# Kernel tuning notes

Measured on AMD Instinct MI355X. Metric: run time of the kernel, lower is better.

Reference implementation:

```python
import jax, jax.numpy as jnp
import numpy as np

EMB = 1024

def setup_inputs() -> dict:
    key = jax.random.key(0)
    ks = jax.random.split(key, 10)
    B, S, E = 8, 2048, EMB
    x = jax.random.normal(ks[0], (B, S, E), dtype=jnp.float32)
    context = jax.random.normal(ks[1], (B, S, E), dtype=jnp.float32)
    pad_mask = jax.random.randint(ks[2], (B, S, S), 0, 2) == 1
    s = 1.0 / np.sqrt(E)
    Wq = jax.random.normal(ks[3], (E, E), dtype=jnp.float32) * s
    bq = jnp.zeros((E,), dtype=jnp.float32)
    Wk = jax.random.normal(ks[4], (E, E), dtype=jnp.float32) * s
    bk = jnp.zeros((E,), dtype=jnp.float32)
    Wv = jax.random.normal(ks[5], (E, E), dtype=jnp.float32) * s
    bv = jnp.zeros((E,), dtype=jnp.float32)
    return {"x": x, "context": context, "pad_mask": pad_mask,
            "Wq": Wq, "bq": bq, "Wk": Wk, "bk": bk, "Wv": Wv, "bv": bv}

def reference(x, context, pad_mask, Wq, bq, Wk, bk, Wv, bv):
    scale = x.shape[-1] ** (-0.5)
    Q = jnp.einsum('bse,fe->bsf', x, Wq) + bq
    K = jnp.einsum('bse,fe->bsf', context, Wk) + bk
    V = jnp.einsum('bse,fe->bsf', context, Wv) + bv
    att = jnp.einsum('bid,bjd->bij', Q, K) * scale
    att = jnp.where(pad_mask, jnp.float32(-1e9), att)
    att = jax.nn.softmax(att, axis=-1)
    out = jnp.einsum('bij,bjk->bik', att, V)
    return (out, att)
```

## Files before the change

kernel.cpp:

```cpp
#include <hip/hip_runtime.h>
#include <hip/hip_bf16.h>
#include <type_traits>

typedef __attribute__((ext_vector_type(8))) __bf16 bf16x8;
typedef __attribute__((ext_vector_type(4))) float f32x4;
typedef unsigned short u16;

__device__ __forceinline__ u16 f2b(float x) {
  union { __hip_bfloat16 b; u16 u; } cv;
  cv.b = __float2bfloat16(x);
  return cv.u;
}

__device__ __forceinline__ void ld16(const u16* g, u16* l) {
  __builtin_amdgcn_global_load_lds(
      (const __attribute__((address_space(1))) unsigned int*)g,
      (__attribute__((address_space(3))) unsigned int*)l, 16, 0, 0);
}

constexpr int BM = 256, BN = 256, BK = 64;

enum { EPI_NONE = 0, EPI_BIAS = 1, EPI_BIAS_T = 2 };

#define PHASE(QR, QC, LA, LB, BUF)                                            \
  {                                                                           \
    if (LA) {                                                                 \
      _Pragma("unroll") for (int i = 0; i < 4; ++i)                           \
          _Pragma("unroll") for (int ks = 0; ks < 2; ++ks)                    \
              aF[i][ks] = *(const bf16x8*)&As[BUF][                           \
                  (wr * 128 + QR * 64 + i * 16 + fr) * BK +                   \
                  (((ks * 4 + quad) ^ (fr & 7)) * 8)];                        \
    }                                                                         \
    if (LB) {                                                                 \
      _Pragma("unroll") for (int j = 0; j < 2; ++j)                           \
          _Pragma("unroll") for (int ks = 0; ks < 2; ++ks)                    \
              bF[j][ks] = *(const bf16x8*)&Bs[BUF][                           \
                  (wc * 64 + QC * 32 + j * 16 + fr) * BK +                    \
                  (((ks * 4 + quad) ^ (fr & 7)) * 8)];                        \
    }                                                                         \
    _Pragma("unroll") for (int i = 0; i < 4; ++i)                             \
        _Pragma("unroll") for (int j = 0; j < 2; ++j)                         \
            _Pragma("unroll") for (int ks = 0; ks < 2; ++ks)                  \
                acc[QR * 4 + i][QC * 2 + j] =                                 \
                    __builtin_amdgcn_mfma_f32_16x16x32_bf16(                  \
                        aF[i][ks], bF[j][ks], acc[QR * 4 + i][QC * 2 + j],    \
                        0, 0, 0);                                             \
  }

template <typename TC, int EPI>
__global__ __launch_bounds__(512, 2) void gemm_bt(
    const u16* __restrict__ A, const u16* __restrict__ Bt, TC* __restrict__ C,
    const float* __restrict__ bias, float scale, int N, int K, long long sA,
    long long sB, long long sC) {
  __shared__ u16 As[2][BM * BK];
  __shared__ u16 Bs[2][BN * BK];

  const int gx = gridDim.x, gy = gridDim.y;
  const int nwg = gx * gy * gridDim.z;
  int flat = (blockIdx.z * gy + blockIdx.y) * gx + blockIdx.x;
  flat = (flat & 7) * (nwg >> 3) + (flat >> 3);
  const int bx = flat % gx;
  const int rem = flat / gx;
  const int by = rem % gy;
  const int bz = rem / gy;

  A += (size_t)bz * sA;
  Bt += (size_t)bz * sB;
  C += (size_t)bz * sC;

  const int m0 = by * BM, n0 = bx * BN;
  const int t = threadIdx.x, wave = t >> 6, lane = t & 63;
  const int wr = wave >> 2, wc = wave & 3;
  const int fr = lane & 15, quad = lane >> 4;
  const int lr = lane >> 3, lc = lane & 7;

  const u16* ga = A + (size_t)(m0 + wave * 8 + lr) * K + (lc ^ lr) * 8;
  const u16* gb = Bt + (size_t)(n0 + wave * 8 + lr) * K + (lc ^ lr) * 8;

  f32x4 acc[8][4] = {};
  bf16x8 aF[4][2], bF[2][2];

  const int nt = K / BK;

  auto STAGE = [&](int kt, int bsel) {
    const size_t ko = (size_t)kt * BK;
#pragma unroll
    for (int i = 0; i < 4; ++i) {
      ld16(ga + (size_t)(i * 64) * K + ko,
           &As[bsel][(i * 64 + wave * 8) * BK]);
      ld16(gb + (size_t)(i * 64) * K + ko,
           &Bs[bsel][(i * 64 + wave * 8) * BK]);
    }
  };

  STAGE(0, 0);
  STAGE(1, 1);

  for (int kt = 0; kt < nt; ++kt) {
    const int b = kt & 1;
    if (kt + 1 < nt)
      __builtin_amdgcn_s_waitcnt(0x0f78);
    else
      __builtin_amdgcn_s_waitcnt(0x0f70);
    __builtin_amdgcn_s_barrier();
    __builtin_amdgcn_sched_barrier(0);

    PHASE(0, 0, 1, 1, b)
    PHASE(0, 1, 0, 1, b)
    PHASE(1, 1, 1, 0, b)
    PHASE(1, 0, 0, 1, b)

    __builtin_amdgcn_sched_barrier(0);
    __builtin_amdgcn_s_barrier();
    if (kt + 2 < nt) STAGE(kt + 2, b);
  }

#pragma unroll
  for (int i = 0; i < 8; ++i)
#pragma unroll
    for (int j = 0; j < 4; ++j) {
      const int mb = m0 + wr * 128 + i * 16 + quad * 4;
      const int n = n0 + wc * 64 + j * 16 + fr;
      if constexpr (EPI == EPI_BIAS_T) {
        const float bb = bias[n];
        const int b = mb >> 11, ml = mb & 2047;
        ushort4 o;
        o.x = f2b(acc[i][j][0] + bb);
        o.y = f2b(acc[i][j][1] + bb);
        o.z = f2b(acc[i][j][2] + bb);
        o.w = f2b(acc[i][j][3] + bb);
        *(ushort4*)&((u16*)C)[(size_t)b * 2097152 + (size_t)n * 2048 + ml] = o;
      } else {
#pragma unroll
        for (int r = 0; r < 4; ++r) {
          const int m = mb + r;
          float v = acc[i][j][r];
          if constexpr (EPI == EPI_BIAS) v += bias[n];
          if constexpr (std::is_same_v<TC, u16>)
            C[(size_t)m * N + n] = f2b(v);
          else
            C[(size_t)m * N + n] = v;
        }
      }
    }
}

__global__ __launch_bounds__(256) void cast_all(
    const float* __restrict__ x, const float* __restrict__ ctx,
    const float* __restrict__ wq, const float* __restrict__ wk,
    const float* __restrict__ wv, u16* __restrict__ xb, u16* __restrict__ cb,
    u16* __restrict__ wqb, u16* __restrict__ wkb, u16* __restrict__ wvb) {
  int b = blockIdx.x;
  const float* s;
  u16* d;
  size_t off;
  if (b < 16384) { s = x; d = xb; off = b; }
  else if (b < 32768) { s = ctx; d = cb; off = b - 32768 + 16384; }
  else if (b < 33792) { s = wq; d = wqb; off = b - 32768; }
  else if (b < 34816) { s = wk; d = wkb; off = b - 33792; }
  else { s = wv; d = wvb; off = b - 34816; }
  const size_t i = (off * 256 + threadIdx.x) * 4;
  float4 v = *(const float4*)&s[i];
  ushort4 h;
  h.x = f2b(v.x); h.y = f2b(v.y); h.z = f2b(v.z); h.w = f2b(v.w);
  *(ushort4*)&d[i] = h;
}

__device__ __forceinline__ float blockReduceMax(float v, float* red) {
#pragma unroll
  for (int o = 32; o > 0; o >>= 1) v = fmaxf(v, __shfl_down(v, o));
  int t = threadIdx.x;
  if ((t & 63) == 0) red[t >> 6] = v;
  __syncthreads();
  float r = fmaxf(fmaxf(red[0], red[1]), fmaxf(red[2], red[3]));
  __syncthreads();
  return r;
}

__device__ __forceinline__ float blockReduceSum(float v, float* red) {
#pragma unroll
  for (int o = 32; o > 0; o >>= 1) v += __shfl_down(v, o);
  int t = threadIdx.x;
  if ((t & 63) == 0) red[t >> 6] = v;
  __syncthreads();
  float r = red[0] + red[1] + red[2] + red[3];
  __syncthreads();
  return r;
}

__global__ __launch_bounds__(256) void softmax_rows(float* __restrict__ att,
                                                    u16* __restrict__ attb,
                                                    const int* __restrict__ msk,
                                                    float scale) {
  __shared__ float red[4];
  float* p = att + (size_t)blockIdx.x * 2048;
  const int* mr = msk + (size_t)blockIdx.x * 2048;
  u16* pb = attb + (size_t)blockIdx.x * 2048;
  const int t = threadIdx.x;
  float4 v0 = ((const float4*)p)[t];
  float4 v1 = ((const float4*)p)[t + 256];
  int4 q0 = ((const int4*)mr)[t];
  int4 q1 = ((const int4*)mr)[t + 256];
  v0.x = q0.x ? -1e9f : v0.x * scale;
  v0.y = q0.y ? -1e9f : v0.y * scale;
  v0.z = q0.z ? -1e9f : v0.z * scale;
  v0.w = q0.w ? -1e9f : v0.w * scale;
  v1.x = q1.x ? -1e9f : v1.x * scale;
  v1.y = q1.y ? -1e9f : v1.y * scale;
  v1.z = q1.z ? -1e9f : v1.z * scale;
  v1.w = q1.w ? -1e9f : v1.w * scale;
  float mx = fmaxf(fmaxf(fmaxf(v0.x, v0.y), fmaxf(v0.z, v0.w)),
                   fmaxf(fmaxf(v1.x, v1.y), fmaxf(v1.z, v1.w)));
  mx = blockReduceMax(mx, red);
  float4 e0, e1;
  e0.x = __expf(v0.x - mx); e0.y = __expf(v0.y - mx);
  e0.z = __expf(v0.z - mx); e0.w = __expf(v0.w - mx);
  e1.x = __expf(v1.x - mx); e1.y = __expf(v1.y - mx);
  e1.z = __expf(v1.z - mx); e1.w = __expf(v1.w - mx);
  float s = (e0.x + e0.y + e0.z + e0.w) + (e1.x + e1.y + e1.z + e1.w);
  s = blockReduceSum(s, red);
  float inv = 1.0f / s;
  e0.x *= inv; e0.y *= inv; e0.z *= inv; e0.w *= inv;
  e1.x *= inv; e1.y *= inv; e1.z *= inv; e1.w *= inv;
  ((float4*)p)[t] = e0;
  ((float4*)p)[t + 256] = e1;
  ushort4 h0, h1;
  h0.x = f2b(e0.x); h0.y = f2b(e0.y); h0.z = f2b(e0.z); h0.w = f2b(e0.w);
  h1.x = f2b(e1.x); h1.y = f2b(e1.y); h1.z = f2b(e1.z); h1.w = f2b(e1.w);
  *(ushort4*)&pb[(size_t)t * 4] = h0;
  *(ushort4*)&pb[(size_t)(t + 256) * 4] = h1;
}

extern "C" void kernel_launch(void* const* d_in, const int* in_sizes, int n_in,
                              void* d_out, int out_size, void* d_ws,
                              size_t ws_size, hipStream_t stream) {
  const float* x   = (const float*)d_in[0];
  const float* ctx = (const float*)d_in[1];
  const int*   msk = (const int*)d_in[2];
  const float* Wq  = (const float*)d_in[3];
  const float* bq  = (const float*)d_in[4];
  const float* Wk  = (const float*)d_in[5];
  const float* bk  = (const float*)d_in[6];
  const float* Wv  = (const float*)d_in[7];
  const float* bv  = (const float*)d_in[8];

  float* out = (float*)d_out;
  float* att = out + 16777216;

  u16* xb = (u16*)d_ws;
  u16* cb = xb + 16777216;
  u16* Q  = cb + 16777216;
  u16* Kb = Q + 16777216;
  u16* Vt = xb;
  u16* attb = Q;
  u16* wqb = (u16*)att;
  u16* wkb = wqb + 1048576;
  u16* wvb = wkb + 1048576;

  dim3 blk(256), blkg(512);
  const long long SQ = 2048LL * 1024, SS = 2048LL * 2048, SV = 1024LL * 2048;

  cast_all<<<dim3(35840), blk, 0, stream>>>(x, ctx, Wq, Wk, Wv, xb, cb, wqb,
                                            wkb, wvb);

  gemm_bt<u16, EPI_BIAS><<<dim3(4, 64, 1), blkg, 0, stream>>>(
      xb, wqb, Q, bq, 0.f, 1024, 1024, 0, 0, 0);
  gemm_bt<u16, EPI_BIAS><<<dim3(4, 64, 1), blkg, 0, stream>>>(
      cb, wkb, Kb, bk, 0.f, 1024, 1024, 0, 0, 0);
  gemm_bt<u16, EPI_BIAS_T><<<dim3(4, 64, 1), blkg, 0, stream>>>(
      cb, wvb, Vt, bv, 0.f, 1024, 1024, 0, 0, 0);

  gemm_bt<float, EPI_NONE><<<dim3(8, 8, 8), blkg, 0, stream>>>(
      Q, Kb, att, nullptr, 0.f, 2048, 1024, SQ, SQ, SS);

  softmax_rows<<<dim3(16384), blk, 0, stream>>>(att, attb, msk, 0.03125f);

  gemm_bt<float, EPI_NONE><<<dim3(4, 8, 8), blkg, 0, stream>>>(
      attb, Vt, out, nullptr, 0.f, 1024, 2048, SS, SV, SQ);
}
```

Baseline: 682.2 us.

## Restructure GEMM inner loop into two halves and batch Q/K projections

Replaces the four-phase fragment schedule with two halves: all B fragments and the first half of A are loaded, MFMAs run, the second half of A is read, and the next tile's global-to-LDS stage is issued before the second MFMA half. This lets the prefetch overlap compute rather than wait until the end of the iteration. Q and K projections are merged into one launch using the z dimension, with a per-batch bias selector. More B fragments are held in registers, which raises register pressure.

```diff
diff --git a/kernel.cpp b/kernel.cpp
--- a/kernel.cpp
+++ b/kernel.cpp
@@ -22,36 +22,11 @@
 
 enum { EPI_NONE = 0, EPI_BIAS = 1, EPI_BIAS_T = 2 };
 
-#define PHASE(QR, QC, LA, LB, BUF)                                            \
-  {                                                                           \
-    if (LA) {                                                                 \
-      _Pragma("unroll") for (int i = 0; i < 4; ++i)                           \
-          _Pragma("unroll") for (int ks = 0; ks < 2; ++ks)                    \
-              aF[i][ks] = *(const bf16x8*)&As[BUF][                           \
-                  (wr * 128 + QR * 64 + i * 16 + fr) * BK +                   \
-                  (((ks * 4 + quad) ^ (fr & 7)) * 8)];                        \
-    }                                                                         \
-    if (LB) {                                                                 \
-      _Pragma("unroll") for (int j = 0; j < 2; ++j)                           \
-          _Pragma("unroll") for (int ks = 0; ks < 2; ++ks)                    \
-              bF[j][ks] = *(const bf16x8*)&Bs[BUF][                           \
-                  (wc * 64 + QC * 32 + j * 16 + fr) * BK +                    \
-                  (((ks * 4 + quad) ^ (fr & 7)) * 8)];                        \
-    }                                                                         \
-    _Pragma("unroll") for (int i = 0; i < 4; ++i)                             \
-        _Pragma("unroll") for (int j = 0; j < 2; ++j)                         \
-            _Pragma("unroll") for (int ks = 0; ks < 2; ++ks)                  \
-                acc[QR * 4 + i][QC * 2 + j] =                                 \
-                    __builtin_amdgcn_mfma_f32_16x16x32_bf16(                  \
-                        aF[i][ks], bF[j][ks], acc[QR * 4 + i][QC * 2 + j],    \
-                        0, 0, 0);                                             \
-  }
-
 template <typename TC, int EPI>
 __global__ __launch_bounds__(512, 2) void gemm_bt(
     const u16* __restrict__ A, const u16* __restrict__ Bt, TC* __restrict__ C,
-    const float* __restrict__ bias, float scale, int N, int K, long long sA,
-    long long sB, long long sC) {
+    const float* __restrict__ bias, const float* __restrict__ bias2, int N,
+    int K, long long sA, long long sB, long long sC) {
   __shared__ u16 As[2][BM * BK];
   __shared__ u16 Bs[2][BN * BK];
 
@@ -67,6 +42,7 @@
   A += (size_t)bz * sA;
   Bt += (size_t)bz * sB;
   C += (size_t)bz * sC;
+  const float* bsel = (bz == 0) ? bias : bias2;
 
   const int m0 = by * BM, n0 = bx * BN;
   const int t = threadIdx.x, wave = t >> 6, lane = t & 63;
@@ -78,18 +54,18 @@
   const u16* gb = Bt + (size_t)(n0 + wave * 8 + lr) * K + (lc ^ lr) * 8;
 
   f32x4 acc[8][4] = {};
-  bf16x8 aF[4][2], bF[2][2];
+  bf16x8 aF[4][2], bF[4][2];
 
   const int nt = K / BK;
 
-  auto STAGE = [&](int kt, int bsel) {
+  auto STAGE = [&](int kt, int bsel2) {
     const size_t ko = (size_t)kt * BK;
 #pragma unroll
     for (int i = 0; i < 4; ++i) {
       ld16(ga + (size_t)(i * 64) * K + ko,
-           &As[bsel][(i * 64 + wave * 8) * BK]);
+           &As[bsel2][(i * 64 + wave * 8) * BK]);
       ld16(gb + (size_t)(i * 64) * K + ko,
-           &Bs[bsel][(i * 64 + wave * 8) * BK]);
+           &Bs[bsel2][(i * 64 + wave * 8) * BK]);
     }
   };
 
@@ -105,14 +81,48 @@
     __builtin_amdgcn_s_barrier();
     __builtin_amdgcn_sched_barrier(0);
 
-    PHASE(0, 0, 1, 1, b)
-    PHASE(0, 1, 0, 1, b)
-    PHASE(1, 1, 1, 0, b)
-    PHASE(1, 0, 0, 1, b)
-
+#pragma unroll
+    for (int i = 0; i < 4; ++i)
+#pragma unroll
+      for (int ks = 0; ks < 2; ++ks)
+        aF[i][ks] = *(const bf16x8*)&As[b][
+            (wr * 128 + i * 16 + fr) * BK + (((ks * 4 + quad) ^ (fr & 7)) * 8)];
+#pragma unroll
+    for (int j = 0; j < 4; ++j)
+#pragma unroll
+      for (int ks = 0; ks < 2; ++ks)
+        bF[j][ks] = *(const bf16x8*)&Bs[b][
+            (wc * 64 + j * 16 + fr) * BK + (((ks * 4 + quad) ^ (fr & 7)) * 8)];
+#pragma unroll
+    for (int i = 0; i < 4; ++i)
+#pragma unroll
+      for (int j = 0; j < 4; ++j)
+#pragma unroll
+        for (int ks = 0; ks < 2; ++ks)
+          acc[i][j] = __builtin_amdgcn_mfma_f32_16x16x32_bf16(
+              aF[i][ks], bF[j][ks], acc[i][j], 0, 0, 0);
+
+#pragma unroll
+    for (int i = 0; i < 4; ++i)
+#pragma unroll
+      for (int ks = 0; ks < 2; ++ks)
+        aF[i][ks] = *(const bf16x8*)&As[b][
+            (wr * 128 + 64 + i * 16 + fr) * BK +
+            (((ks * 4 + quad) ^ (fr & 7)) * 8)];
+    __builtin_amdgcn_s_waitcnt(0xc07f);
     __builtin_amdgcn_sched_barrier(0);
     __builtin_amdgcn_s_barrier();
+    __builtin_amdgcn_sched_barrier(0);
     if (kt + 2 < nt) STAGE(kt + 2, b);
+
+#pragma unroll
+    for (int i = 0; i < 4; ++i)
+#pragma unroll
+      for (int j = 0; j < 4; ++j)
+#pragma unroll
+        for (int ks = 0; ks < 2; ++ks)
+          acc[i + 4][j] = __builtin_amdgcn_mfma_f32_16x16x32_bf16(
+              aF[i][ks], bF[j][ks], acc[i + 4][j], 0, 0, 0);
   }
 
 #pragma unroll
@@ -122,20 +132,21 @@
       const int mb = m0 + wr * 128 + i * 16 + quad * 4;
       const int n = n0 + wc * 64 + j * 16 + fr;
       if constexpr (EPI == EPI_BIAS_T) {
-        const float bb = bias[n];
-        const int b = mb >> 11, ml = mb & 2047;
+        const float bb = bsel[n];
+        const int bb2 = mb >> 11, ml = mb & 2047;
         ushort4 o;
         o.x = f2b(acc[i][j][0] + bb);
         o.y = f2b(acc[i][j][1] + bb);
         o.z = f2b(acc[i][j][2] + bb);
         o.w = f2b(acc[i][j][3] + bb);
-        *(ushort4*)&((u16*)C)[(size_t)b * 2097152 + (size_t)n * 2048 + ml] = o;
+        *(ushort4*)&((u16*)C)[(size_t)bb2 * 2097152 + (size_t)n * 2048 + ml] =
+            o;
       } else {
 #pragma unroll
         for (int r = 0; r < 4; ++r) {
           const int m = mb + r;
           float v = acc[i][j][r];
-          if constexpr (EPI == EPI_BIAS) v += bias[n];
+          if constexpr (EPI == EPI_BIAS) v += bsel[n];
           if constexpr (std::is_same_v<TC, u16>)
             C[(size_t)m * N + n] = f2b(v);
           else
@@ -263,18 +274,16 @@
   cast_all<<<dim3(35840), blk, 0, stream>>>(x, ctx, Wq, Wk, Wv, xb, cb, wqb,
                                             wkb, wvb);
 
-  gemm_bt<u16, EPI_BIAS><<<dim3(4, 64, 1), blkg, 0, stream>>>(
-      xb, wqb, Q, bq, 0.f, 1024, 1024, 0, 0, 0);
-  gemm_bt<u16, EPI_BIAS><<<dim3(4, 64, 1), blkg, 0, stream>>>(
-      cb, wkb, Kb, bk, 0.f, 1024, 1024, 0, 0, 0);
+  gemm_bt<u16, EPI_BIAS><<<dim3(4, 64, 2), blkg, 0, stream>>>(
+      xb, wqb, Q, bq, bk, 1024, 1024, 16777216LL, 1048576LL, 16777216LL);
   gemm_bt<u16, EPI_BIAS_T><<<dim3(4, 64, 1), blkg, 0, stream>>>(
-      cb, wvb, Vt, bv, 0.f, 1024, 1024, 0, 0, 0);
+      cb, wvb, Vt, bv, bv, 1024, 1024, 0, 0, 0);
 
   gemm_bt<float, EPI_NONE><<<dim3(8, 8, 8), blkg, 0, stream>>>(
-      Q, Kb, att, nullptr, 0.f, 2048, 1024, SQ, SQ, SS);
+      Q, Kb, att, nullptr, nullptr, 2048, 1024, SQ, SQ, SS);
 
   softmax_rows<<<dim3(16384), blk, 0, stream>>>(att, attb, msk, 0.03125f);
 
   gemm_bt<float, EPI_NONE><<<dim3(4, 8, 8), blkg, 0, stream>>>(
-      attb, Vt, out, nullptr, 0.f, 1024, 2048, SS, SV, SQ);
-}
+      attb, Vt, out, nullptr, nullptr, 1024, 2048, SS, SV, SQ);
+}
```

After: 668.6 us. 2.0% less time.
